# Optimization experiments

Hardware: AMD Instinct MI355X
Metric: run time of the kernel (lower is better)

The kernel has to match this reference:

```python
import jax, jax.numpy as jnp
import numpy as np

SEL_TEMP = 0.001
NORM_TEMP = 7.0


def setup_inputs() -> dict:
    key = jax.random.key(0)
    k1, k2 = jax.random.split(key)
    B, L, F = 32, 128, 64
    x = jax.random.uniform(k1, (B, L, F), dtype=jnp.float32)
    # nn.Parameter(torch.rand(F, F, F, F+1))
    interaction = jax.random.uniform(k2, (F, F, F, F + 1), dtype=jnp.float32)
    return {"x": x, "interaction": interaction}


def _step(interaction, T, s):
    # s: [B,F] state, T: [B,F,F] transition, interaction: [F,F,F,F+1]
    ns = jnp.concatenate([s[:, :, None], T], axis=2)          # [B,F,F+1]
    # candidate[b,i,j,k] = sum_m interaction[i,j,m,k] * ns[b,m,k]
    cand = jnp.einsum('ijmk,bmk->bijk', interaction, ns)      # [B,F,F,F+1]
    hi = jax.nn.softmax(s / SEL_TEMP, axis=1)                 # [B,F]
    lo = jax.nn.softmax(1.0 - s / SEL_TEMP, axis=1)           # [B,F]
    # sum over i,j of cand[b,i,j,k]*hi[b,j]*lo[b,i] without materializing tfs
    scores = jnp.einsum('bijk,bj,bi->bk', cand, hi, lo)       # [B,F+1]
    sw = jax.nn.softmax(scores / SEL_TEMP, axis=1)            # [B,F+1]
    sel = jnp.einsum('bijk,bk->bij', cand, sw)                # [B,F,F]
    sel = jax.nn.softmax(sel * NORM_TEMP, axis=1)             # softmax over rows (dim=1)
    new_s = jnp.einsum('bij,bj->bi', sel, s)                  # [B,F]
    return new_s, sel


def reference(x, interaction):
    B, L, F = x.shape
    T0 = jnp.full((B, F, F), 1.0 / F, dtype=x.dtype)  # softmax of zeros

    def scan_body(T, s):
        new_s, sel = _step(interaction, T, s)
        return sel, new_s

    x_t = jnp.swapaxes(x, 0, 1)                        # [L,B,F]
    T_final, outs = jax.lax.scan(scan_body, T0, x_t)   # outs: [L,B,F]
    return jnp.swapaxes(outs, 0, 1), T_final
```

## Files before the change

### kernel.cpp

```cpp
#include <hip/hip_runtime.h>
#include <math.h>

#define FF 64
#define FP1 65
#define BB 32
#define LL 128
#define NBL 4096
#define NIJ 4096

typedef __attribute__((ext_vector_type(8))) short short8;
typedef __attribute__((ext_vector_type(4))) float f32x4;

__device__ __forceinline__ unsigned short f2b(float f) {
    union { float f; unsigned u; } v; v.f = f;
    unsigned r = v.u + 0x7fffu + ((v.u >> 16) & 1u);
    return (unsigned short)(r >> 16);
}
__device__ __forceinline__ float b2f(unsigned short h) {
    union { unsigned u; float f; } v; v.u = ((unsigned)h) << 16; return v.f;
}

#define OFF_BH   0ull
#define OFF_BL   524288ull
#define OFF_FLAG 1048576ull
#define WS_NEED  1048640ull

__global__ void build_slabB(const float* __restrict__ inter,
                            unsigned short* __restrict__ bH,
                            unsigned short* __restrict__ bL,
                            int* __restrict__ flag) {
    const size_t t = (size_t)blockIdx.x * 256 + threadIdx.x;
    if (t == 0) *flag = 0;
    const int e = (int)(t & 7);
    const int lane = (int)((t >> 3) & 63);
    const int fn = (int)((t >> 9) & 255);
    const int ks = (int)(t >> 17);
    const int n = fn * 16 + (lane & 15);
    const int i = n & 63;
    const int j = n >> 6;
    const int m = ks * 32 + ((lane >> 4) & 3) * 8 + e;
    const float v = inter[((size_t)(i * FF + j) * FF + m) * FP1];
    const unsigned short h = f2b(v);
    bH[t] = h;
    bL[t] = f2b(v - b2f(h));
}

__launch_bounds__(512)
__global__ void fused_mfma(const float* __restrict__ x,
                           const unsigned short* __restrict__ bH,
                           const unsigned short* __restrict__ bL,
                           float* __restrict__ out,
                           int* __restrict__ flag) {
    __shared__ float xT[FF][17];
    __shared__ float part[8][FF][17];
    __shared__ float wmn[8];

    const int tid = threadIdx.x;
    const int w = tid >> 6, lane = tid & 63;
    const int fm = blockIdx.x;
    const int bl0 = fm * 16;
    const int hi4 = lane >> 4;
    const int c15 = lane & 15;

    for (int idx = tid; idx < 1024; idx += 512) {
        const int bl_local = idx >> 6, j = idx & 63;
        xT[j][bl_local] = x[(size_t)(bl0 + bl_local) * FF + j];
    }

    short8 aH[2], aL[2];
    #pragma unroll
    for (int ks = 0; ks < 2; ++ks) {
        const float* xp = x + (size_t)(bl0 + c15) * FF + ks * 32 + hi4 * 8;
        const float4 v0 = *(const float4*)xp;
        const float4 v1 = *(const float4*)(xp + 4);
        float vv[8] = {v0.x, v0.y, v0.z, v0.w, v1.x, v1.y, v1.z, v1.w};
        unsigned short hh[8], ll[8];
        #pragma unroll
        for (int e = 0; e < 8; ++e) {
            hh[e] = f2b(vv[e]);
            ll[e] = f2b(vv[e] - b2f(hh[e]));
        }
        aH[ks] = *(const short8*)hh;
        aL[ks] = *(const short8*)ll;
    }
    __syncthreads();

    f32x4 racc[4];
    #pragma unroll
    for (int q = 0; q < 4; ++q) racc[q] = (f32x4){0.f, 0.f, 0.f, 0.f};
    f32x4 mn4 = (f32x4){INFINITY, INFINITY, INFINITY, INFINITY};

    const bool wrT = ((fm & 7) == 7) && (hi4 == 3);
    float* out1 = out + (size_t)BB * LL * FF + (size_t)(fm >> 3) * NIJ;

    #pragma unroll 1
    for (int jj = 0; jj < 8; ++jj) {
        const int j = w * 8 + jj;
        f32x4 acc[4];
        #pragma unroll
        for (int q = 0; q < 4; ++q) acc[q] = (f32x4){0.f, 0.f, 0.f, 0.f};
        #pragma unroll
        for (int ks = 0; ks < 2; ++ks) {
            #pragma unroll
            for (int q = 0; q < 4; ++q) {
                const size_t bb = (((size_t)ks * 256 + j * 4 + q) * 64 + lane) * 8;
                const short8 bHf = *(const short8*)(bH + bb);
                const short8 bLf = *(const short8*)(bL + bb);
                acc[q] = __builtin_amdgcn_mfma_f32_16x16x32_bf16(aH[ks], bHf, acc[q], 0, 0, 0);
                acc[q] = __builtin_amdgcn_mfma_f32_16x16x32_bf16(aH[ks], bLf, acc[q], 0, 0, 0);
                acc[q] = __builtin_amdgcn_mfma_f32_16x16x32_bf16(aL[ks], bHf, acc[q], 0, 0, 0);
            }
        }
        f32x4 z[4], mxv;
        #pragma unroll
        for (int q = 0; q < 4; ++q) {
            z[q] = acc[q] * 7.0f;
            #pragma unroll
            for (int c = 0; c < 4; ++c) mn4[c] = fminf(mn4[c], z[q][c]);
        }
        #pragma unroll
        for (int c = 0; c < 4; ++c)
            mxv[c] = fmaxf(fmaxf(z[0][c], z[1][c]), fmaxf(z[2][c], z[3][c]));
        #pragma unroll
        for (int o = 1; o < 16; o <<= 1)
            #pragma unroll
            for (int c = 0; c < 4; ++c) mxv[c] = fmaxf(mxv[c], __shfl_xor(mxv[c], o));
        f32x4 e[4], s = (f32x4){0.f, 0.f, 0.f, 0.f};
        #pragma unroll
        for (int q = 0; q < 4; ++q) {
            #pragma unroll
            for (int c = 0; c < 4; ++c) e[q][c] = __expf(z[q][c] - mxv[c]);
            s += e[q];
        }
        #pragma unroll
        for (int o = 1; o < 16; o <<= 1)
            #pragma unroll
            for (int c = 0; c < 4; ++c) s[c] += __shfl_xor(s[c], o);
        f32x4 inv;
        #pragma unroll
        for (int c = 0; c < 4; ++c) inv[c] = 1.0f / s[c];
        f32x4 xbv;
        #pragma unroll
        for (int c = 0; c < 4; ++c) xbv[c] = xT[j][hi4 * 4 + c];
        #pragma unroll
        for (int q = 0; q < 4; ++q) {
            const f32x4 wq = e[q] * inv;
            racc[q] += wq * xbv;
            if (wrT) out1[(q * 16 + c15) * 64 + j] = wq[3];
        }
    }

    #pragma unroll
    for (int q = 0; q < 4; ++q)
        #pragma unroll
        for (int r = 0; r < 4; ++r)
            part[w][q * 16 + c15][hi4 * 4 + r] = racc[q][r];

    float mn = fminf(fminf(mn4[0], mn4[1]), fminf(mn4[2], mn4[3]));
    #pragma unroll
    for (int o = 1; o < 64; o <<= 1) mn = fminf(mn, __shfl_xor(mn, o));
    if (lane == 0) wmn[w] = mn;
    __syncthreads();

    for (int idx = tid; idx < 1024; idx += 512) {
        const int bl_local = idx >> 6, i = idx & 63;
        float a = 0.f;
        #pragma unroll
        for (int ww = 0; ww < 8; ++ww) a += part[ww][i][bl_local];
        out[(size_t)(bl0 + bl_local) * FF + i] = a;
    }
    if (tid == 0) {
        float m2 = wmn[0];
        #pragma unroll
        for (int ww = 1; ww < 8; ++ww) m2 = fminf(m2, wmn[ww]);
        if (!(m2 >= 10.5f)) atomicOr(flag, 1);
    }
}

__global__ void build_slab0(const float* __restrict__ inter, float* __restrict__ slab0T) {
    int t = blockIdx.x * blockDim.x + threadIdx.x;
    if (t < FF * FF * FF) {
        int m = t >> 12;
        int ij = t & 4095;
        slab0T[t] = inter[((size_t)ij * FF + m) * FP1];
    }
}

__launch_bounds__(1024, 1)
__global__ void coil_main(const float* __restrict__ x,
                          const float* __restrict__ inter,
                          const float* __restrict__ slab0T,
                          float* __restrict__ out,
                          int useSlab,
                          const int* __restrict__ flag) {
    if (flag && *flag == 0) return;

    __shared__ float Tlds[FF][FP1];
    __shared__ float selr[FF][FP1];
    __shared__ float s_l[FF], hiW[FF], loW[FF];
    __shared__ float zsc[FP1], swW[FP1], scoresAcc[FP1];
    __shared__ float chunkA[8][FP1 + 3];
    __shared__ int IL[FF], JL[FF];
    __shared__ int nIJ[2];
    __shared__ int Klist[FP1];
    __shared__ float Kw[FP1];
    __shared__ int nK;
    __shared__ float redmx;

    const int b = blockIdx.x;
    const int tid = threadIdx.x;
    const int wave = tid >> 6;
    const int lane = tid & 63;

    for (int idx = tid; idx < FF * FP1; idx += 1024)
        ((float*)Tlds)[idx] = 1.0f / FF;

    const float* xb = x + (size_t)b * LL * FF;
    float* out0 = out + (size_t)b * LL * FF;
    float* out1 = out + (size_t)BB * LL * FF + (size_t)b * FF * FF;

    for (int l = 0; l < LL; ++l) {
        __syncthreads();
        if (tid < FF) s_l[tid] = xb[l * FF + tid];
        __syncthreads();
        if (wave == 0) {
            float z = s_l[lane] / 0.001f;
            float mx = z;
            for (int o = 32; o > 0; o >>= 1) mx = fmaxf(mx, __shfl_xor(mx, o));
            float e = expf(z - mx);
            float sm = e;
            for (int o = 32; o > 0; o >>= 1) sm += __shfl_xor(sm, o);
            float w = e / sm;
            hiW[lane] = w;
            unsigned long long msk = __ballot(w > 1e-16f);
            int pos = (int)__popcll(msk & ((1ull << lane) - 1ull));
            if (w > 1e-16f) JL[pos] = lane;
            if (lane == 0) nIJ[1] = (int)__popcll(msk);
        } else if (wave == 1) {
            float z = 1.0f - s_l[lane] / 0.001f;
            float mx = z;
            for (int o = 32; o > 0; o >>= 1) mx = fmaxf(mx, __shfl_xor(mx, o));
            float e = expf(z - mx);
            float sm = e;
            for (int o = 32; o > 0; o >>= 1) sm += __shfl_xor(sm, o);
            float w = e / sm;
            loW[lane] = w;
            unsigned long long msk = __ballot(w > 1e-16f);
            int pos = (int)__popcll(msk & ((1ull << lane) - 1ull));
            if (w > 1e-16f) IL[pos] = lane;
            if (lane == 0) nIJ[0] = (int)__popcll(msk);
        }
        if (tid < FP1) scoresAcc[tid] = 0.0f;
        __syncthreads();

        const int nI = nIJ[0], nJ = nIJ[1];
        const int npairs = nI * nJ;
        for (int pbase = 0; pbase < npairs; pbase += 8) {
            int prem = npairs - pbase; if (prem > 8) prem = 8;
            int p_local = wave >> 1, half = wave & 1;
            if (p_local < prem) {
                int p = pbase + p_local;
                int i = IL[p / nJ];
                int jx = JL[p % nJ];
                float vv = loW[i] * hiW[jx];
                int k = half * 32 + lane;
                bool act = half ? (lane < 33) : (lane < 32);
                if (act) {
                    const float* base = inter + (size_t)(i * FF + jx) * (FF * FP1) + k;
                    const float* nsv = (k == 0) ? s_l : &Tlds[k - 1][0];
                    float acc = 0.0f;
                    #pragma unroll 16
                    for (int m = 0; m < FF; ++m) acc += base[m * FP1] * nsv[m];
                    chunkA[p_local][k] = vv * acc;
                }
            }
            __syncthreads();
            if (tid < FP1) {
                float a = scoresAcc[tid];
                for (int pl = 0; pl < prem; ++pl) a += chunkA[pl][tid];
                scoresAcc[tid] = a;
            }
            __syncthreads();
        }
        if (tid < FP1) zsc[tid] = scoresAcc[tid] / 0.001f;
        __syncthreads();
        if (tid == 0) {
            float mx = zsc[0];
            for (int k = 1; k < FP1; ++k) mx = fmaxf(mx, zsc[k]);
            redmx = mx;
        }
        __syncthreads();
        if (tid < FP1) zsc[tid] = expf(zsc[tid] - redmx);
        __syncthreads();
        if (tid == 0) {
            float sm = 0.0f;
            for (int k = 0; k < FP1; ++k) sm += zsc[k];
            int cnt = 0;
            for (int k = 0; k < FP1; ++k) {
                float w = zsc[k] / sm;
                swW[k] = w;
                if (w > 1e-14f) { Klist[cnt] = k; Kw[cnt] = w; ++cnt; }
            }
            nK = cnt;
        }
        __syncthreads();

        float ax = 0.f, ay = 0.f, az = 0.f, aw = 0.f;
        const int ij0 = tid * 4;
        for (int kk = 0; kk < nK; ++kk) {
            int k = Klist[kk];
            float wk = Kw[kk];
            float dx = 0.f, dy = 0.f, dz = 0.f, dw = 0.f;
            if (k == 0 && useSlab) {
                const float4* sp = (const float4*)slab0T;
                #pragma unroll 8
                for (int m = 0; m < FF; ++m) {
                    float4 f = sp[m * (FF * FF / 4) + tid];
                    float ns = s_l[m];
                    dx += f.x * ns; dy += f.y * ns; dz += f.z * ns; dw += f.w * ns;
                }
            } else {
                const float* nsv = (k == 0) ? s_l : &Tlds[k - 1][0];
                const float* bp = inter + (size_t)ij0 * (FF * FP1) + k;
                #pragma unroll 8
                for (int m = 0; m < FF; ++m) {
                    float ns = nsv[m];
                    dx += bp[m * FP1] * ns;
                    dy += bp[m * FP1 + FF * FP1] * ns;
                    dz += bp[m * FP1 + 2 * FF * FP1] * ns;
                    dw += bp[m * FP1 + 3 * FF * FP1] * ns;
                }
            }
            ax += wk * dx; ay += wk * dy; az += wk * dz; aw += wk * dw;
        }
        {
            int ii = tid >> 4;
            int jj = (tid & 15) * 4;
            selr[jj + 0][ii] = ax; selr[jj + 1][ii] = ay;
            selr[jj + 2][ii] = az; selr[jj + 3][ii] = aw;
        }
        __syncthreads();
        if (tid < FF) {
            int jcol = tid;
            float mx = -INFINITY;
            for (int i2 = 0; i2 < FF; ++i2) mx = fmaxf(mx, selr[jcol][i2] * 7.0f);
            float sm = 0.0f;
            for (int i2 = 0; i2 < FF; ++i2) {
                float e = expf(selr[jcol][i2] * 7.0f - mx);
                selr[jcol][i2] = e; sm += e;
            }
            for (int i2 = 0; i2 < FF; ++i2) Tlds[jcol][i2] = selr[jcol][i2] / sm;
        }
        __syncthreads();
        if (tid < FF) {
            float acc2 = 0.0f;
            for (int j2 = 0; j2 < FF; ++j2) acc2 += Tlds[j2][tid] * s_l[j2];
            out0[l * FF + tid] = acc2;
        }
    }
    __syncthreads();
    for (int idx = tid; idx < FF * FF; idx += 1024) {
        int i2 = idx >> 6, j2 = idx & 63;
        out1[idx] = Tlds[j2][i2];
    }
}

extern "C" void kernel_launch(void* const* d_in, const int* in_sizes, int n_in,
                              void* d_out, int out_size, void* d_ws, size_t ws_size,
                              hipStream_t stream) {
    const float* x = (const float*)d_in[0];
    const float* inter = (const float*)d_in[1];
    float* outp = (float*)d_out;
    char* ws = (char*)d_ws;

    if (ws_size >= WS_NEED) {
        unsigned short* bH = (unsigned short*)(ws + OFF_BH);
        unsigned short* bL = (unsigned short*)(ws + OFF_BL);
        int* flag = (int*)(ws + OFF_FLAG);

        build_slabB<<<dim3(1024), dim3(256), 0, stream>>>(inter, bH, bL, flag);
        fused_mfma<<<dim3(256), dim3(512), 0, stream>>>(x, bH, bL, outp, flag);
        coil_main<<<dim3(BB), dim3(1024), 0, stream>>>(x, inter, (const float*)0, outp, 0, flag);
    } else {
        float* slab0T = (float*)ws;
        int useSlab = (ws_size >= (size_t)FF * FF * FF * sizeof(float)) ? 1 : 0;
        if (useSlab)
            build_slab0<<<dim3(1024), dim3(256), 0, stream>>>(inter, slab0T);
        coil_main<<<dim3(BB), dim3(1024), 0, stream>>>(x, inter, slab0T, outp, useSlab, (const int*)0);
    }
}
```

Baseline: 34.81 us.

## Process two 16-row M fragments per block to reuse B fragment loads

Each fused_mfma block now handles 32 (b,l) rows instead of 16, so every bH/bL fragment loaded from global memory feeds MFMAs for two A fragments. The grid is halved to 128 blocks and the shared-memory tiles grow to 33 columns. This halves B-operand traffic per output row. In exchange it raises register pressure and leaves fewer blocks than the GPU has compute units, which lowers parallelism.

```diff
diff --git a/kernel.cpp b/kernel.cpp
--- a/kernel.cpp
+++ b/kernel.cpp
@@ -45,60 +45,68 @@
     bL[t] = f2b(v - b2f(h));
 }
 
-__launch_bounds__(512)
+__launch_bounds__(512, 2)
 __global__ void fused_mfma(const float* __restrict__ x,
                            const unsigned short* __restrict__ bH,
                            const unsigned short* __restrict__ bL,
                            float* __restrict__ out,
                            int* __restrict__ flag) {
-    __shared__ float xT[FF][17];
-    __shared__ float part[8][FF][17];
+    __shared__ float xT[FF][33];
+    __shared__ float part[8][FF][33];
     __shared__ float wmn[8];
 
     const int tid = threadIdx.x;
     const int w = tid >> 6, lane = tid & 63;
     const int fm = blockIdx.x;
-    const int bl0 = fm * 16;
+    const int bl0 = fm * 32;
     const int hi4 = lane >> 4;
     const int c15 = lane & 15;
 
-    for (int idx = tid; idx < 1024; idx += 512) {
+    #pragma unroll
+    for (int p = 0; p < 4; ++p) {
+        const int idx = tid + p * 512;
         const int bl_local = idx >> 6, j = idx & 63;
         xT[j][bl_local] = x[(size_t)(bl0 + bl_local) * FF + j];
     }
 
-    short8 aH[2], aL[2];
-    #pragma unroll
-    for (int ks = 0; ks < 2; ++ks) {
-        const float* xp = x + (size_t)(bl0 + c15) * FF + ks * 32 + hi4 * 8;
-        const float4 v0 = *(const float4*)xp;
-        const float4 v1 = *(const float4*)(xp + 4);
-        float vv[8] = {v0.x, v0.y, v0.z, v0.w, v1.x, v1.y, v1.z, v1.w};
-        unsigned short hh[8], ll[8];
-        #pragma unroll
-        for (int e = 0; e < 8; ++e) {
-            hh[e] = f2b(vv[e]);
-            ll[e] = f2b(vv[e] - b2f(hh[e]));
-        }
-        aH[ks] = *(const short8*)hh;
-        aL[ks] = *(const short8*)ll;
-    }
+    short8 aH[2][2], aL[2][2];
+    #pragma unroll
+    for (int mf = 0; mf < 2; ++mf)
+        #pragma unroll
+        for (int ks = 0; ks < 2; ++ks) {
+            const float* xp = x + (size_t)(bl0 + mf * 16 + c15) * FF + ks * 32 + hi4 * 8;
+            const float4 v0 = *(const float4*)xp;
+            const float4 v1 = *(const float4*)(xp + 4);
+            float vv[8] = {v0.x, v0.y, v0.z, v0.w, v1.x, v1.y, v1.z, v1.w};
+            unsigned short hh[8], ll[8];
+            #pragma unroll
+            for (int e = 0; e < 8; ++e) {
+                hh[e] = f2b(vv[e]);
+                ll[e] = f2b(vv[e] - b2f(hh[e]));
+            }
+            aH[mf][ks] = *(const short8*)hh;
+            aL[mf][ks] = *(const short8*)ll;
+        }
     __syncthreads();
 
-    f32x4 racc[4];
-    #pragma unroll
-    for (int q = 0; q < 4; ++q) racc[q] = (f32x4){0.f, 0.f, 0.f, 0.f};
+    f32x4 racc[2][4];
+    #pragma unroll
+    for (int mf = 0; mf < 2; ++mf)
+        #pragma unroll
+        for (int q = 0; q < 4; ++q) racc[mf][q] = (f32x4){0.f, 0.f, 0.f, 0.f};
     f32x4 mn4 = (f32x4){INFINITY, INFINITY, INFINITY, INFINITY};
 
-    const bool wrT = ((fm & 7) == 7) && (hi4 == 3);
-    float* out1 = out + (size_t)BB * LL * FF + (size_t)(fm >> 3) * NIJ;
+    const bool wrT = ((fm & 3) == 3) && (hi4 == 3);
+    float* out1 = out + (size_t)BB * LL * FF + (size_t)(fm >> 2) * NIJ;
 
     #pragma unroll 1
     for (int jj = 0; jj < 8; ++jj) {
         const int j = w * 8 + jj;
-        f32x4 acc[4];
-        #pragma unroll
-        for (int q = 0; q < 4; ++q) acc[q] = (f32x4){0.f, 0.f, 0.f, 0.f};
+        f32x4 acc[2][4];
+        #pragma unroll
+        for (int mf = 0; mf < 2; ++mf)
+            #pragma unroll
+            for (int q = 0; q < 4; ++q) acc[mf][q] = (f32x4){0.f, 0.f, 0.f, 0.f};
         #pragma unroll
         for (int ks = 0; ks < 2; ++ks) {
             #pragma unroll
@@ -106,55 +114,62 @@
                 const size_t bb = (((size_t)ks * 256 + j * 4 + q) * 64 + lane) * 8;
                 const short8 bHf = *(const short8*)(bH + bb);
                 const short8 bLf = *(const short8*)(bL + bb);
-                acc[q] = __builtin_amdgcn_mfma_f32_16x16x32_bf16(aH[ks], bHf, acc[q], 0, 0, 0);
-                acc[q] = __builtin_amdgcn_mfma_f32_16x16x32_bf16(aH[ks], bLf, acc[q], 0, 0, 0);
-                acc[q] = __builtin_amdgcn_mfma_f32_16x16x32_bf16(aL[ks], bHf, acc[q], 0, 0, 0);
-            }
-        }
-        f32x4 z[4], mxv;
-        #pragma unroll
-        for (int q = 0; q < 4; ++q) {
-            z[q] = acc[q] * 7.0f;
-            #pragma unroll
-            for (int c = 0; c < 4; ++c) mn4[c] = fminf(mn4[c], z[q][c]);
-        }
-        #pragma unroll
-        for (int c = 0; c < 4; ++c)
-            mxv[c] = fmaxf(fmaxf(z[0][c], z[1][c]), fmaxf(z[2][c], z[3][c]));
-        #pragma unroll
-        for (int o = 1; o < 16; o <<= 1)
-            #pragma unroll
-            for (int c = 0; c < 4; ++c) mxv[c] = fmaxf(mxv[c], __shfl_xor(mxv[c], o));
-        f32x4 e[4], s = (f32x4){0.f, 0.f, 0.f, 0.f};
-        #pragma unroll
-        for (int q = 0; q < 4; ++q) {
-            #pragma unroll
-            for (int c = 0; c < 4; ++c) e[q][c] = __expf(z[q][c] - mxv[c]);
-            s += e[q];
-        }
-        #pragma unroll
-        for (int o = 1; o < 16; o <<= 1)
-            #pragma unroll
-            for (int c = 0; c < 4; ++c) s[c] += __shfl_xor(s[c], o);
-        f32x4 inv;
-        #pragma unroll
-        for (int c = 0; c < 4; ++c) inv[c] = 1.0f / s[c];
-        f32x4 xbv;
-        #pragma unroll
-        for (int c = 0; c < 4; ++c) xbv[c] = xT[j][hi4 * 4 + c];
-        #pragma unroll
-        for (int q = 0; q < 4; ++q) {
-            const f32x4 wq = e[q] * inv;
-            racc[q] += wq * xbv;
-            if (wrT) out1[(q * 16 + c15) * 64 + j] = wq[3];
-        }
-    }
-
-    #pragma unroll
-    for (int q = 0; q < 4; ++q)
-        #pragma unroll
-        for (int r = 0; r < 4; ++r)
-            part[w][q * 16 + c15][hi4 * 4 + r] = racc[q][r];
+                #pragma unroll
+                for (int mf = 0; mf < 2; ++mf) {
+                    acc[mf][q] = __builtin_amdgcn_mfma_f32_16x16x32_bf16(aH[mf][ks], bHf, acc[mf][q], 0, 0, 0);
+                    acc[mf][q] = __builtin_amdgcn_mfma_f32_16x16x32_bf16(aH[mf][ks], bLf, acc[mf][q], 0, 0, 0);
+                    acc[mf][q] = __builtin_amdgcn_mfma_f32_16x16x32_bf16(aL[mf][ks], bHf, acc[mf][q], 0, 0, 0);
+                }
+            }
+        }
+        #pragma unroll
+        for (int mf = 0; mf < 2; ++mf) {
+            f32x4 z[4], mxv;
+            #pragma unroll
+            for (int q = 0; q < 4; ++q) {
+                z[q] = acc[mf][q] * 7.0f;
+                #pragma unroll
+                for (int c = 0; c < 4; ++c) mn4[c] = fminf(mn4[c], z[q][c]);
+            }
+            #pragma unroll
+            for (int c = 0; c < 4; ++c)
+                mxv[c] = fmaxf(fmaxf(z[0][c], z[1][c]), fmaxf(z[2][c], z[3][c]));
+            #pragma unroll
+            for (int o = 1; o < 16; o <<= 1)
+                #pragma unroll
+                for (int c = 0; c < 4; ++c) mxv[c] = fmaxf(mxv[c], __shfl_xor(mxv[c], o));
+            f32x4 e[4], s = (f32x4){0.f, 0.f, 0.f, 0.f};
+            #pragma unroll
+            for (int q = 0; q < 4; ++q) {
+                #pragma unroll
+                for (int c = 0; c < 4; ++c) e[q][c] = __expf(z[q][c] - mxv[c]);
+                s += e[q];
+            }
+            #pragma unroll
+            for (int o = 1; o < 16; o <<= 1)
+                #pragma unroll
+                for (int c = 0; c < 4; ++c) s[c] += __shfl_xor(s[c], o);
+            f32x4 inv, xbv;
+            #pragma unroll
+            for (int c = 0; c < 4; ++c) inv[c] = 1.0f / s[c];
+            #pragma unroll
+            for (int c = 0; c < 4; ++c) xbv[c] = xT[j][mf * 16 + hi4 * 4 + c];
+            #pragma unroll
+            for (int q = 0; q < 4; ++q) {
+                const f32x4 wq = e[q] * inv;
+                racc[mf][q] += wq * xbv;
+                if (wrT && mf == 1) out1[(q * 16 + c15) * 64 + j] = wq[3];
+            }
+        }
+    }
+
+    #pragma unroll
+    for (int mf = 0; mf < 2; ++mf)
+        #pragma unroll
+        for (int q = 0; q < 4; ++q)
+            #pragma unroll
+            for (int r = 0; r < 4; ++r)
+                part[w][q * 16 + c15][mf * 16 + hi4 * 4 + r] = racc[mf][q][r];
 
     float mn = fminf(fminf(mn4[0], mn4[1]), fminf(mn4[2], mn4[3]));
     #pragma unroll
@@ -162,7 +177,9 @@
     if (lane == 0) wmn[w] = mn;
     __syncthreads();
 
-    for (int idx = tid; idx < 1024; idx += 512) {
+    #pragma unroll
+    for (int p = 0; p < 4; ++p) {
+        const int idx = tid + p * 512;
         const int bl_local = idx >> 6, i = idx & 63;
         float a = 0.f;
         #pragma unroll
@@ -379,7 +396,7 @@
         int* flag = (int*)(ws + OFF_FLAG);
 
         build_slabB<<<dim3(1024), dim3(256), 0, stream>>>(inter, bH, bL, flag);
-        fused_mfma<<<dim3(256), dim3(512), 0, stream>>>(x, bH, bL, outp, flag);
+        fused_mfma<<<dim3(128), dim3(512), 0, stream>>>(x, bH, bL, outp, flag);
         coil_main<<<dim3(BB), dim3(1024), 0, stream>>>(x, inter, (const float*)0, outp, 0, flag);
     } else {
         float* slab0T = (float*)ws;
```

New measurement: 41.79 us. +20.1%, slower.
